# Kernel tuning notes

Measured on AMD Instinct MI355X. Metric: run time of the kernel, lower is better.

Reference implementation:

```python
import jax, jax.numpy as jnp
import numpy as np

B, S, HID = 2, 2048, 2048
H, KVH, D = 32, 4, 128
EPS = 1e-6
ROPE_THETA = 1e6
INIT = 0.02


def setup_inputs() -> dict:
    key = jax.random.key(0)
    ks = jax.random.split(key, 6)
    hidden_states = jax.random.normal(ks[0], (B, S, HID), jnp.float32)
    q_w = jax.random.normal(ks[1], (HID, H * D), jnp.float32) * INIT
    k_w = jax.random.normal(ks[2], (HID, KVH * D), jnp.float32) * INIT
    v_w = jax.random.normal(ks[3], (HID, KVH * D), jnp.float32) * INIT
    o_w = jax.random.normal(ks[4], (H * D, HID), jnp.float32) * INIT
    q_norm_w = jnp.ones((D,), jnp.float32)
    k_norm_w = jnp.ones((D,), jnp.float32)
    # rotary embeddings, computed once per position (B, S, D)
    pos = jnp.arange(S, dtype=jnp.float32)
    inv_freq = 1.0 / (ROPE_THETA ** (jnp.arange(0, D, 2, dtype=jnp.float32) / D))
    freqs = pos[:, None] * inv_freq[None, :]          # (S, D/2)
    emb = jnp.concatenate([freqs, freqs], axis=-1)    # (S, D)
    cos = jnp.broadcast_to(jnp.cos(emb)[None], (B, S, D))
    sin = jnp.broadcast_to(jnp.sin(emb)[None], (B, S, D))
    # causal mask (is_causal=True, sliding_window=None)
    attn_mask = jnp.tril(jnp.ones((S, S), bool))[None, None]  # (1,1,S,S)
    return {"hidden_states": hidden_states, "cos": cos, "sin": sin,
            "q_w": q_w, "k_w": k_w, "v_w": v_w, "o_w": o_w,
            "q_norm_w": q_norm_w, "k_norm_w": k_norm_w, "attn_mask": attn_mask}


def _rms_norm(x, w):
    xf = x.astype(jnp.float32)
    var = jnp.mean(jax.lax.square(xf), axis=-1, keepdims=True)
    return (w * (xf * jax.lax.rsqrt(var + EPS))).astype(x.dtype)


def _rotate_half(x):
    x1, x2 = jnp.split(x, 2, axis=-1)
    return jnp.concatenate([-x2, x1], axis=-1)


def _apply_rope(q, k, cos, sin):
    # q: (B,H,S,D), k: (B,KVH,S,D); cos/sin: (B,S,D) -> (B,1,S,D)
    cos = cos[:, None]
    sin = sin[:, None]
    q = q * cos + _rotate_half(q) * sin
    k = k * cos + _rotate_half(k) * sin
    return q, k


def reference(hidden_states, cos, sin, q_w, k_w, v_w, o_w, q_norm_w, k_norm_w, attn_mask):
    b, s, _ = hidden_states.shape
    scaling = D ** (-0.5)
    # projections + per-head QK RMSNorm
    q = _rms_norm((hidden_states @ q_w).reshape(b, s, H, D), q_norm_w)
    k = _rms_norm((hidden_states @ k_w).reshape(b, s, KVH, D), k_norm_w)
    v = (hidden_states @ v_w).reshape(b, s, KVH, D)
    q = jnp.transpose(q, (0, 2, 1, 3))   # (b,H,s,D)
    k = jnp.transpose(k, (0, 2, 1, 3))   # (b,KVH,s,D)
    v = jnp.transpose(v, (0, 2, 1, 3))
    q, k = _apply_rope(q, k, cos, sin)
    # GQA: repeat KV heads across groups
    groups = H // KVH
    k = jnp.repeat(k, groups, axis=1)    # (b,H,s,D)
    v = jnp.repeat(v, groups, axis=1)
    # eager softmax attention (fp32 softmax)
    scores = jnp.einsum('bhqd,bhkd->bhqk', q, k).astype(jnp.float32) * scaling
    scores = jnp.where(attn_mask, scores, jnp.float32(-1e30))
    probs = jax.nn.softmax(scores, axis=-1).astype(q.dtype)
    attn = jnp.einsum('bhqk,bhkd->bhqd', probs, v)
    attn = jnp.transpose(attn, (0, 2, 1, 3)).reshape(b, s, H * D)
    return attn @ o_w
```

## Files before the change

### kernel.cpp

```cpp
#include <hip/hip_runtime.h>
#include <hip/hip_bf16.h>

typedef unsigned short u16;
typedef __attribute__((ext_vector_type(4))) float f32x4;
typedef __attribute__((ext_vector_type(16))) float f32x16;
typedef __attribute__((ext_vector_type(8))) short bf16x8;
typedef __attribute__((ext_vector_type(4))) unsigned u32x4;

#define B_ 2
#define S_ 2048
#define HID_ 2048
#define H_ 32
#define KVH_ 4
#define D_ 128
#define M_ 4096
#define NQ_ 4096
#define NKV_ 512

typedef const __attribute__((address_space(1))) void gconst_void;
typedef __attribute__((address_space(3))) void lds_void;

static __device__ __forceinline__ void gload_lds16(const void* g, void* l) {
  __builtin_amdgcn_global_load_lds((gconst_void*)g, (lds_void*)l, 16, 0, 0);
}

static __device__ __forceinline__ u16 f2b(float f) {
  union { float f; unsigned i; } x; x.f = f;
  return (u16)((x.i + 0x7fffu + ((x.i >> 16) & 1u)) >> 16);
}
static __device__ __forceinline__ float b2f(u16 u) {
  union { unsigned i; float f; } x; x.i = ((unsigned)u) << 16;
  return x.f;
}

__global__ void k_cvt(const float* __restrict__ in, u16* __restrict__ out, int n4) {
  int i = blockIdx.x * blockDim.x + threadIdx.x;
  int stride = gridDim.x * blockDim.x;
  for (; i < n4; i += stride) {
    float4 v = reinterpret_cast<const float4*>(in)[i];
    ushort4 o;
    o.x = f2b(v.x); o.y = f2b(v.y); o.z = f2b(v.z); o.w = f2b(v.w);
    reinterpret_cast<ushort4*>(out)[i] = o;
  }
}

__global__ __launch_bounds__(256) void k_transpose(const float* __restrict__ W,
                                                   u16* __restrict__ Wt, int K, int N) {
  __shared__ u16 t[64][72];
  int n0 = blockIdx.x * 64, k0 = blockIdx.y * 64;
  int tid = threadIdx.x;
  int r = tid >> 4;
  int c4 = (tid & 15) * 4;
#pragma unroll
  for (int i = 0; i < 4; i++) {
    int k = r + i * 16;
    float4 v = *reinterpret_cast<const float4*>(W + (size_t)(k0 + k) * N + n0 + c4);
    t[k][c4 + 0] = f2b(v.x); t[k][c4 + 1] = f2b(v.y);
    t[k][c4 + 2] = f2b(v.z); t[k][c4 + 3] = f2b(v.w);
  }
  __syncthreads();
#pragma unroll
  for (int i = 0; i < 4; i++) {
    int n = r + i * 16;
    ushort4 o;
    o.x = t[c4 + 0][n]; o.y = t[c4 + 1][n]; o.z = t[c4 + 2][n]; o.w = t[c4 + 3][n];
    *reinterpret_cast<ushort4*>(Wt + (size_t)(n0 + n) * K + k0 + c4) = o;
  }
}

__device__ __forceinline__ void gemm_core(const u16* __restrict__ A, const u16* __restrict__ Bt,
                                          int K, int m0, int n0,
                                          u16* As, u16* Bs, f32x4 (&acc)[4][4]) {
  const int tid = threadIdx.x;
  const int lane = tid & 63;
  const int wid = tid >> 6;
  const int wr = wid >> 1, wc = wid & 1;
  const int lrow = lane & 15;
  const int hi = lane >> 4;
  const f32x4 zz = {0.f, 0.f, 0.f, 0.f};
#pragma unroll
  for (int i = 0; i < 4; i++)
#pragma unroll
    for (int j = 0; j < 4; j++) acc[i][j] = zz;

  const int srow = tid >> 3;
  const int sc16 = tid & 7;
  const int nk = K >> 6;
  int cur = 0;

#pragma unroll
  for (int rep = 0; rep < 4; rep++) {
    int row = rep * 32 + srow;
    int gcol = ((sc16 ^ (row & 7)) << 3);
    gload_lds16(A + (size_t)(m0 + row) * K + gcol, As + row * 64 + sc16 * 8);
    gload_lds16(Bt + (size_t)(n0 + row) * K + gcol, Bs + row * 64 + sc16 * 8);
  }
  __syncthreads();

  for (int t = 0; t < nk; t++) {
    if (t + 1 < nk) {
      int nxt = cur ^ 1;
      int kb = (t + 1) << 6;
#pragma unroll
      for (int rep = 0; rep < 4; rep++) {
        int row = rep * 32 + srow;
        int gcol = kb + ((sc16 ^ (row & 7)) << 3);
        gload_lds16(A + (size_t)(m0 + row) * K + gcol, As + nxt * 8192 + row * 64 + sc16 * 8);
        gload_lds16(Bt + (size_t)(n0 + row) * K + gcol, Bs + nxt * 8192 + row * 64 + sc16 * 8);
      }
    }
    const u16* Ac = As + cur * 8192;
    const u16* Bc = Bs + cur * 8192;
#pragma unroll
    for (int kc = 0; kc < 2; kc++) {
      bf16x8 af[4], bfr[4];
#pragma unroll
      for (int i = 0; i < 4; i++) {
        int row = wr * 64 + i * 16 + lrow;
        af[i] = *reinterpret_cast<const bf16x8*>(Ac + row * 64 + ((((kc << 2) + hi) ^ (row & 7)) << 3));
      }
#pragma unroll
      for (int j = 0; j < 4; j++) {
        int row = wc * 64 + j * 16 + lrow;
        bfr[j] = *reinterpret_cast<const bf16x8*>(Bc + row * 64 + ((((kc << 2) + hi) ^ (row & 7)) << 3));
      }
#pragma unroll
      for (int i = 0; i < 4; i++)
#pragma unroll
        for (int j = 0; j < 4; j++)
          acc[i][j] = __builtin_amdgcn_mfma_f32_16x16x32_bf16(af[i], bfr[j], acc[i][j], 0, 0, 0);
    }
    __syncthreads();
    cur ^= 1;
  }
}

__global__ __launch_bounds__(256, 2) void k_gemm_qkv(const u16* __restrict__ hb,
    const u16* __restrict__ qwt, const u16* __restrict__ kwt, const u16* __restrict__ vwt,
    u16* __restrict__ qb, u16* __restrict__ kb, u16* __restrict__ vb) {
  __shared__ u16 As[2 * 128 * 64], Bs[2 * 128 * 64];
  int mt = blockIdx.x, nt = blockIdx.y;
  const u16* Bt;
  if (nt < 32)      Bt = qwt;
  else if (nt < 36) Bt = kwt;
  else              Bt = vwt;
  int head = (nt < 32) ? nt : ((nt < 36) ? nt - 32 : nt - 36);
  f32x4 acc[4][4];
  gemm_core(hb, Bt, HID_, mt * 128, head * 128, As, Bs, acc);
  const int lane = threadIdx.x & 63;
  const int wid = threadIdx.x >> 6;
  const int wr = wid >> 1, wc = wid & 1;
  const int lr4 = (lane >> 4) * 4, lc = lane & 15;
#pragma unroll
  for (int i = 0; i < 4; i++)
#pragma unroll
    for (int j = 0; j < 4; j++)
#pragma unroll
      for (int r = 0; r < 4; r++) {
        int m = mt * 128 + wr * 64 + i * 16 + lr4 + r;
        int d = wc * 64 + j * 16 + lc;
        int b = m >> 11, s = m & (S_ - 1);
        u16 val = f2b(acc[i][j][r]);
        if (nt < 32) {
          qb[(((size_t)b * H_ + head) * S_ + s) * D_ + d] = val;
        } else if (nt < 36) {
          kb[(((size_t)b * KVH_ + head) * S_ + s) * D_ + d] = val;
        } else {
          vb[(((size_t)b * KVH_ + head) * D_ + d) * S_ + s] = val;
        }
      }
}

__global__ __launch_bounds__(256, 2) void k_gemm_o(const u16* __restrict__ ab,
    const u16* __restrict__ owt, float* __restrict__ out) {
  __shared__ u16 As[2 * 128 * 64], Bs[2 * 128 * 64];
  int mt = blockIdx.x, nt = blockIdx.y;
  f32x4 acc[4][4];
  gemm_core(ab, owt, NQ_, mt * 128, nt * 128, As, Bs, acc);
  const int lane = threadIdx.x & 63;
  const int wid = threadIdx.x >> 6;
  const int wr = wid >> 1, wc = wid & 1;
  const int lr4 = (lane >> 4) * 4, lc = lane & 15;
#pragma unroll
  for (int i = 0; i < 4; i++)
#pragma unroll
    for (int j = 0; j < 4; j++)
#pragma unroll
      for (int r = 0; r < 4; r++) {
        int m = mt * 128 + wr * 64 + i * 16 + lr4 + r;
        int n = nt * 128 + wc * 64 + j * 16 + lc;
        out[(size_t)m * HID_ + n] = acc[i][j][r];
      }
}

__global__ __launch_bounds__(256) void k_norm_rope(u16* __restrict__ qb, u16* __restrict__ kb,
    const float* __restrict__ cosp, const float* __restrict__ sinp,
    const float* __restrict__ qnw, const float* __restrict__ knw) {
  int row = blockIdx.x * 4 + (threadIdx.x >> 6);
  int lane = threadIdx.x & 63;
  const int QROWS = B_ * H_ * S_;
  u16* ptr; const float* nw; int b, s;
  if (row < QROWS) {
    ptr = qb + (size_t)row * D_; nw = qnw;
    s = row & (S_ - 1); b = row / (H_ * S_);
  } else {
    int r2 = row - QROWS;
    ptr = kb + (size_t)r2 * D_; nw = knw;
    s = r2 & (S_ - 1); b = r2 / (KVH_ * S_);
  }
  int d = lane * 2;
  float x0 = b2f(ptr[d]), x1 = b2f(ptr[d + 1]);
  float ss = x0 * x0 + x1 * x1;
#pragma unroll
  for (int m = 1; m < 64; m <<= 1) ss += __shfl_xor(ss, m);
  float inv = rsqrtf(ss * (1.0f / 128.0f) + 1e-6f);
  x0 = x0 * inv * nw[d]; x1 = x1 * inv * nw[d + 1];
  float p0 = __shfl_xor(x0, 32), p1 = __shfl_xor(x1, 32);
  float r0 = (lane < 32) ? -p0 : p0;
  float r1 = (lane < 32) ? -p1 : p1;
  const float* cp = cosp + ((size_t)b * S_ + s) * D_;
  const float* sp = sinp + ((size_t)b * S_ + s) * D_;
  ptr[d]     = f2b(x0 * cp[d]     + r0 * sp[d]);
  ptr[d + 1] = f2b(x1 * cp[d + 1] + r1 * sp[d + 1]);
}

__global__ __launch_bounds__(512, 2) void k_attn(const u16* __restrict__ q,
    const u16* __restrict__ k, const u16* __restrict__ vt, u16* __restrict__ out) {
  __shared__ u16 Kb[2 * 64 * 128];
  __shared__ u16 Vb[2 * 128 * 64];
  const int bh = blockIdx.y;
  const int b = bh >> 5, h = bh & 31;
  const int kvh = h >> 3;
  const int tid = threadIdx.x, lane = tid & 63, w = tid >> 6;
  const int lq = lane & 31, hi = lane >> 5;
  const u16* qp  = q  + ((size_t)(b * H_ + h) * S_) * D_;
  const u16* kp  = k  + ((size_t)(b * KVH_ + kvh) * S_) * D_;
  const u16* vtp = vt + ((size_t)(b * KVH_ + kvh) * D_) * S_;

  const int rowKa = tid >> 4;
  const int colK  = ((tid & 15) ^ (rowKa & 15)) << 3;
  const int rowVa = tid >> 3;
  const int colV  = ((tid & 7) ^ (rowVa & 7)) << 3;

  const float KSC = 0.08838834764831845f * 1.44269504088896340f;
  const f32x16 z16 = {0.f};

  int cur = 0;
  for (int half = 0; half < 2; half++) {
    const int qt = half ? (7 - (int)blockIdx.x) : (int)blockIdx.x;
    const int q0 = qt * 256;
    const int last = 4 * qt + 3;
    const int qg = q0 + 32 * w + lq;

    {
      u16* kd = Kb + cur * 8192 + tid * 8;
      u16* vd = Vb + cur * 8192 + tid * 8;
      gload_lds16(kp + (size_t)rowKa * D_ + colK, kd);
      gload_lds16(kp + (size_t)(rowKa + 32) * D_ + colK, kd + 4096);
      gload_lds16(vtp + (size_t)rowVa * S_ + colV, vd);
      gload_lds16(vtp + (size_t)(rowVa + 64) * S_ + colV, vd + 4096);
    }

    bf16x8 qf[8];
#pragma unroll
    for (int ds = 0; ds < 8; ds++)
      qf[ds] = *reinterpret_cast<const bf16x8*>(qp + (size_t)qg * D_ + ds * 16 + hi * 8);

    f32x16 oacc[4];
#pragma unroll
    for (int dt = 0; dt < 4; dt++) oacc[dt] = z16;
    float mrun = -1e30f, lrun = 0.f;

    __syncthreads();

    for (int nt = 0; nt <= last; nt++) {
      const int n0 = nt * 64;
      if (nt < last) {
        const int n1 = n0 + 64;
        u16* kd = Kb + (cur ^ 1) * 8192 + tid * 8;
        u16* vd = Vb + (cur ^ 1) * 8192 + tid * 8;
        gload_lds16(kp + (size_t)(n1 + rowKa) * D_ + colK, kd);
        gload_lds16(kp + (size_t)(n1 + rowKa + 32) * D_ + colK, kd + 4096);
        gload_lds16(vtp + (size_t)rowVa * S_ + n1 + colV, vd);
        gload_lds16(vtp + (size_t)(rowVa + 64) * S_ + n1 + colV, vd + 4096);
      }
      const u16* Kc = Kb + cur * 8192;
      const u16* Vc = Vb + cur * 8192;

      const bool skip = (n0 > q0 + 32 * w + 31);
      if (!skip) {
        const bool needmask = (n0 + 63 > q0 + 32 * w);

        f32x16 sacc[2];
        sacc[0] = z16; sacc[1] = z16;
#pragma unroll
        for (int ds = 0; ds < 8; ds++) {
          const int sl = (((ds << 1) + hi) ^ (lq & 15)) << 3;
          bf16x8 ka0 = *reinterpret_cast<const bf16x8*>(Kc + lq * 128 + sl);
          bf16x8 ka1 = *reinterpret_cast<const bf16x8*>(Kc + (lq + 32) * 128 + sl);
          __builtin_amdgcn_s_setprio(1);
          sacc[0] = __builtin_amdgcn_mfma_f32_32x32x16_bf16(ka0, qf[ds], sacc[0], 0, 0, 0);
          sacc[1] = __builtin_amdgcn_mfma_f32_32x32x16_bf16(ka1, qf[ds], sacc[1], 0, 0, 0);
          __builtin_amdgcn_s_setprio(0);
        }

        float tm = -1e30f;
#pragma unroll
        for (int t = 0; t < 2; t++)
#pragma unroll
          for (int r = 0; r < 16; r++) {
            float s2 = sacc[t][r] * KSC;
            if (needmask) {
              int kvg = n0 + 32 * t + (r & 3) + 8 * (r >> 2) + 4 * hi;
              if (kvg > qg) s2 = -1e30f;
            }
            sacc[t][r] = s2;
            tm = fmaxf(tm, s2);
          }
        tm = fmaxf(tm, __shfl_xor(tm, 32));
        if (__any(tm > mrun + 8.f)) {
          float mn = fmaxf(mrun, tm);
          float al = exp2f(mrun - mn);
          mrun = mn;
          lrun *= al;
#pragma unroll
          for (int r = 0; r < 16; r++) {
            float ar = __shfl(al, (r & 3) + 8 * (r >> 2) + 4 * hi);
#pragma unroll
            for (int dt = 0; dt < 4; dt++) oacc[dt][r] *= ar;
          }
        }
        float rs = 0.f;
#pragma unroll
        for (int t = 0; t < 2; t++)
#pragma unroll
          for (int r = 0; r < 16; r++) {
            float pv = exp2f(sacc[t][r] - mrun);
            sacc[t][r] = pv;
            rs += pv;
          }
        rs += __shfl_xor(rs, 32);
        lrun += rs;

        u32x4 pa[4];
#pragma unroll
        for (int t = 0; t < 2; t++)
#pragma unroll
          for (int ksl = 0; ksl < 2; ksl++) {
            unsigned wa, wb, wc2, wd;
            asm("v_cvt_pk_bf16_f32 %0, %1, %2" : "=v"(wa)
                : "v"(sacc[t][8 * ksl + 0]), "v"(sacc[t][8 * ksl + 1]));
            asm("v_cvt_pk_bf16_f32 %0, %1, %2" : "=v"(wb)
                : "v"(sacc[t][8 * ksl + 2]), "v"(sacc[t][8 * ksl + 3]));
            asm("v_cvt_pk_bf16_f32 %0, %1, %2" : "=v"(wc2)
                : "v"(sacc[t][8 * ksl + 4]), "v"(sacc[t][8 * ksl + 5]));
            asm("v_cvt_pk_bf16_f32 %0, %1, %2" : "=v"(wd)
                : "v"(sacc[t][8 * ksl + 6]), "v"(sacc[t][8 * ksl + 7]));
            asm("v_permlane32_swap_b32 %0, %1" : "+v"(wa), "+v"(wc2));
            asm("v_permlane32_swap_b32 %0, %1" : "+v"(wb), "+v"(wd));
            u32x4 t4 = {wa, wb, wc2, wd};
            pa[t * 2 + ksl] = t4;
          }

#pragma unroll
        for (int ks = 0; ks < 4; ks++) {
          bf16x8 paf = __builtin_bit_cast(bf16x8, pa[ks]);
          bf16x8 bv[4];
#pragma unroll
          for (int dt = 0; dt < 4; dt++) {
            int rowv = dt * 32 + lq;
            bv[dt] = *reinterpret_cast<const bf16x8*>(
                Vc + rowv * 64 + ((((ks << 1) + hi) ^ (rowv & 7)) << 3));
          }
          __builtin_amdgcn_s_setprio(1);
#pragma unroll
          for (int dt = 0; dt < 4; dt++)
            oacc[dt] = __builtin_amdgcn_mfma_f32_32x32x16_bf16(paf, bv[dt], oacc[dt], 0, 0, 0);
          __builtin_amdgcn_s_setprio(0);
        }
      }
      __syncthreads();
      cur ^= 1;
    }

    float linv = 1.0f / lrun;
#pragma unroll
    for (int r = 0; r < 16; r++) {
      const int idx_r = (r & 3) + 8 * (r >> 2) + 4 * hi;
      float lr = __shfl(linv, idx_r);
      size_t base = ((size_t)b * S_ + (q0 + 32 * w + idx_r)) * NQ_ + h * D_ + lq;
#pragma unroll
      for (int dt = 0; dt < 4; dt++)
        out[base + dt * 32] = f2b(oacc[dt][r] * lr);
    }
  }
}

extern "C" void kernel_launch(void* const* d_in, const int* in_sizes, int n_in,
                              void* d_out, int out_size, void* d_ws, size_t ws_size,
                              hipStream_t stream) {
  const float* hidden = (const float*)d_in[0];
  const float* cosp   = (const float*)d_in[1];
  const float* sinp   = (const float*)d_in[2];
  const float* q_w    = (const float*)d_in[3];
  const float* k_w    = (const float*)d_in[4];
  const float* v_w    = (const float*)d_in[5];
  const float* o_w    = (const float*)d_in[6];
  const float* qnw    = (const float*)d_in[7];
  const float* knw    = (const float*)d_in[8];

  char* p = (char*)d_ws;
  u16* hb  = (u16*)p; p += (size_t)M_ * HID_ * 2;
  u16* qwt = (u16*)p; p += (size_t)NQ_ * HID_ * 2;
  u16* kwt = (u16*)p; p += (size_t)NKV_ * HID_ * 2;
  u16* vwt = (u16*)p; p += (size_t)NKV_ * HID_ * 2;
  u16* owt = (u16*)p; p += (size_t)HID_ * NQ_ * 2;
  u16* qb  = (u16*)p; p += (size_t)B_ * H_ * S_ * D_ * 2;
  u16* kb  = (u16*)p; p += (size_t)B_ * KVH_ * S_ * D_ * 2;
  u16* vb  = (u16*)p; p += (size_t)B_ * KVH_ * S_ * D_ * 2;
  u16* ab  = (u16*)p; p += (size_t)M_ * NQ_ * 2;

  k_cvt<<<2048, 256, 0, stream>>>(hidden, hb, M_ * HID_ / 4);
  k_transpose<<<dim3(NQ_ / 64, HID_ / 64), 256, 0, stream>>>(q_w, qwt, HID_, NQ_);
  k_transpose<<<dim3(NKV_ / 64, HID_ / 64), 256, 0, stream>>>(k_w, kwt, HID_, NKV_);
  k_transpose<<<dim3(NKV_ / 64, HID_ / 64), 256, 0, stream>>>(v_w, vwt, HID_, NKV_);
  k_transpose<<<dim3(HID_ / 64, NQ_ / 64), 256, 0, stream>>>(o_w, owt, NQ_, HID_);
  k_gemm_qkv<<<dim3(M_ / 128, 40), 256, 0, stream>>>(hb, qwt, kwt, vwt, qb, kb, vb);
  k_norm_rope<<<(B_ * H_ * S_ + B_ * KVH_ * S_) / 4, 256, 0, stream>>>(qb, kb, cosp, sinp, qnw, knw);
  k_attn<<<dim3(4, B_ * H_), 512, 0, stream>>>(qb, kb, vb, ab);
  k_gemm_o<<<dim3(M_ / 128, HID_ / 128), 256, 0, stream>>>(ab, owt, (float*)d_out);
}
```

Baseline: 371.8 us.

## Add 256x256 8-wave Q-projection GEMM and XCD-aware block remapping

Moves the Q projection out of the combined QKV GEMM into a dedicated kernel. It uses 256x256 tiles, 512 threads, quadrant-wise LDS double buffering with explicit waitcnt and barriers, and MFMA priority boosting, so each loaded tile is reused across more output. K/V projection stays in its own smaller kernel. The QKV, attention and output-projection grids become 1D with a swizzle that maps consecutive blocks onto the same XCD, aiming to improve L2 locality. The cost is more kernel launches, higher register and LDS pressure in the new GEMM, and delicate hand-tuned vmcnt synchronization.

```diff
diff --git a/kernel.cpp b/kernel.cpp
--- a/kernel.cpp
+++ b/kernel.cpp
@@ -23,6 +23,9 @@
 static __device__ __forceinline__ void gload_lds16(const void* g, void* l) {
   __builtin_amdgcn_global_load_lds((gconst_void*)g, (lds_void*)l, 16, 0, 0);
 }
+
+#define WAITV(N) asm volatile("s_waitcnt vmcnt(" #N ")" ::: "memory")
+#define WAITL0() asm volatile("s_waitcnt lgkmcnt(0)" ::: "memory")
 
 static __device__ __forceinline__ u16 f2b(float f) {
   union { float f; unsigned i; } x; x.f = f;
@@ -135,16 +138,145 @@
   }
 }
 
-__global__ __launch_bounds__(256, 2) void k_gemm_qkv(const u16* __restrict__ hb,
-    const u16* __restrict__ qwt, const u16* __restrict__ kwt, const u16* __restrict__ vwt,
-    u16* __restrict__ qb, u16* __restrict__ kb, u16* __restrict__ vb) {
+__global__ __launch_bounds__(512, 2) void k_gemm_q8(const u16* __restrict__ A,
+    const u16* __restrict__ Bt, u16* __restrict__ qb) {
+  __shared__ u16 Ash[2][2][128 * 64];
+  __shared__ u16 Bsh[2][2][128 * 64];
+  const int bid = blockIdx.x;
+  const int wg = (bid & 7) * 32 + (bid >> 3);
+  const int mt = wg & 15, nt = wg >> 4;
+  const int m0 = mt * 256, n0 = nt * 256;
+  const int K = HID_, nk = K >> 6;
+  const int tid = threadIdx.x, lane = tid & 63;
+  const int wv = tid >> 6, wr = wv >> 2, wc = wv & 3;
+  const int lrow = lane & 15, hi4 = lane >> 4;
+
+  const int s0r = tid >> 3, sc = tid & 7;
+  const int s1r = (tid + 512) >> 3;
+
+  auto stgA = [&](int h, int t, int d) {
+    gload_lds16(A + (size_t)(m0 + h * 128 + s0r) * K + t * 64 + ((sc ^ (s0r & 7)) << 3),
+                &Ash[d][h][s0r * 64 + sc * 8]);
+    gload_lds16(A + (size_t)(m0 + h * 128 + s1r) * K + t * 64 + ((sc ^ (s1r & 7)) << 3),
+                &Ash[d][h][s1r * 64 + sc * 8]);
+  };
+  auto stgB = [&](int h, int t, int d) {
+    gload_lds16(Bt + (size_t)(n0 + h * 128 + s0r) * K + t * 64 + ((sc ^ (s0r & 7)) << 3),
+                &Bsh[d][h][s0r * 64 + sc * 8]);
+    gload_lds16(Bt + (size_t)(n0 + h * 128 + s1r) * K + t * 64 + ((sc ^ (s1r & 7)) << 3),
+                &Bsh[d][h][s1r * 64 + sc * 8]);
+  };
+
+  f32x4 acc[8][4];
+  const f32x4 zz = {0.f, 0.f, 0.f, 0.f};
+#pragma unroll
+  for (int f = 0; f < 8; f++)
+#pragma unroll
+    for (int j = 0; j < 4; j++) acc[f][j] = zz;
+
+  bf16x8 af[4][2], bfr[2][2];
+
+  auto lda = [&](int mh, int d) {
+#pragma unroll
+    for (int fi = 0; fi < 4; fi++) {
+      int row = fi * 32 + wr * 16 + lrow;
+#pragma unroll
+      for (int kk = 0; kk < 2; kk++)
+        af[fi][kk] = *reinterpret_cast<const bf16x8*>(
+            &Ash[d][mh][row * 64 + ((((kk << 2) + hi4) ^ (row & 7)) << 3)]);
+    }
+  };
+  auto ldb = [&](int nh, int d) {
+#pragma unroll
+    for (int ji = 0; ji < 2; ji++) {
+      int row = ji * 64 + wc * 16 + lrow;
+#pragma unroll
+      for (int kk = 0; kk < 2; kk++)
+        bfr[ji][kk] = *reinterpret_cast<const bf16x8*>(
+            &Bsh[d][nh][row * 64 + ((((kk << 2) + hi4) ^ (row & 7)) << 3)]);
+    }
+  };
+  auto mq = [&](int mh, int nh) {
+    __builtin_amdgcn_s_setprio(1);
+#pragma unroll
+    for (int kk = 0; kk < 2; kk++)
+#pragma unroll
+      for (int fi = 0; fi < 4; fi++)
+#pragma unroll
+        for (int ji = 0; ji < 2; ji++)
+          acc[mh * 4 + fi][nh * 2 + ji] = __builtin_amdgcn_mfma_f32_16x16x32_bf16(
+              af[fi][kk], bfr[ji][kk], acc[mh * 4 + fi][nh * 2 + ji], 0, 0, 0);
+    __builtin_amdgcn_s_setprio(0);
+  };
+
+  stgA(0, 0, 0); stgB(0, 0, 0); stgA(1, 0, 0); stgB(1, 0, 0);
+  WAITV(0);
+  __builtin_amdgcn_s_barrier();
+
+  for (int t = 0; t < nk; t++) {
+    const int d = t & 1, nd = d ^ 1;
+    const bool pre = (t + 1 < nk);
+    if (pre) { stgA(0, t + 1, nd); stgB(0, t + 1, nd); }
+    lda(0, d); ldb(0, d);
+    WAITV(6);
+    __builtin_amdgcn_sched_barrier(0);
+    __builtin_amdgcn_s_barrier();
+    WAITL0();
+    __builtin_amdgcn_sched_barrier(0);
+    mq(0, 0);
+    __builtin_amdgcn_s_barrier();
+    if (pre) stgA(1, t + 1, nd);
+    lda(1, d);
+    WAITV(6);
+    __builtin_amdgcn_sched_barrier(0);
+    __builtin_amdgcn_s_barrier();
+    WAITL0();
+    __builtin_amdgcn_sched_barrier(0);
+    mq(1, 0);
+    __builtin_amdgcn_s_barrier();
+    if (pre) stgB(1, t + 1, nd);
+    ldb(1, d);
+    __builtin_amdgcn_sched_barrier(0);
+    __builtin_amdgcn_s_barrier();
+    WAITL0();
+    __builtin_amdgcn_sched_barrier(0);
+    mq(1, 1);
+    __builtin_amdgcn_s_barrier();
+    lda(0, d);
+    WAITV(4);
+    __builtin_amdgcn_sched_barrier(0);
+    __builtin_amdgcn_s_barrier();
+    WAITL0();
+    __builtin_amdgcn_sched_barrier(0);
+    mq(0, 1);
+    __builtin_amdgcn_s_barrier();
+  }
+
+  const int lr4 = hi4 * 4, lc = lane & 15;
+#pragma unroll
+  for (int f = 0; f < 8; f++)
+#pragma unroll
+    for (int j = 0; j < 4; j++)
+#pragma unroll
+      for (int rr = 0; rr < 4; rr++) {
+        int m = m0 + f * 32 + wr * 16 + lr4 + rr;
+        int ncol = n0 + j * 64 + wc * 16 + lc;
+        int b = m >> 11, s = m & (S_ - 1);
+        int head = ncol >> 7, dd = ncol & 127;
+        qb[(((size_t)b * H_ + head) * S_ + s) * D_ + dd] = f2b(acc[f][j][rr]);
+      }
+}
+
+__global__ __launch_bounds__(256, 2) void k_gemm_kv(const u16* __restrict__ hb,
+    const u16* __restrict__ kwt, const u16* __restrict__ vwt,
+    u16* __restrict__ kb, u16* __restrict__ vb) {
   __shared__ u16 As[2 * 128 * 64], Bs[2 * 128 * 64];
-  int mt = blockIdx.x, nt = blockIdx.y;
-  const u16* Bt;
-  if (nt < 32)      Bt = qwt;
-  else if (nt < 36) Bt = kwt;
-  else              Bt = vwt;
-  int head = (nt < 32) ? nt : ((nt < 36) ? nt - 32 : nt - 36);
+  const int bid = blockIdx.x;
+  const int wg = (bid & 7) * 32 + (bid >> 3);
+  const int mt = wg & 31, nt = wg >> 5;
+  const bool isv = nt >= 4;
+  const int head = isv ? nt - 4 : nt;
+  const u16* Bt = isv ? vwt : kwt;
   f32x4 acc[4][4];
   gemm_core(hb, Bt, HID_, mt * 128, head * 128, As, Bs, acc);
   const int lane = threadIdx.x & 63;
@@ -161,20 +293,17 @@
         int d = wc * 64 + j * 16 + lc;
         int b = m >> 11, s = m & (S_ - 1);
         u16 val = f2b(acc[i][j][r]);
-        if (nt < 32) {
-          qb[(((size_t)b * H_ + head) * S_ + s) * D_ + d] = val;
-        } else if (nt < 36) {
-          kb[(((size_t)b * KVH_ + head) * S_ + s) * D_ + d] = val;
-        } else {
-          vb[(((size_t)b * KVH_ + head) * D_ + d) * S_ + s] = val;
-        }
+        if (isv) vb[(((size_t)b * KVH_ + head) * D_ + d) * S_ + s] = val;
+        else     kb[(((size_t)b * KVH_ + head) * S_ + s) * D_ + d] = val;
       }
 }
 
 __global__ __launch_bounds__(256, 2) void k_gemm_o(const u16* __restrict__ ab,
     const u16* __restrict__ owt, float* __restrict__ out) {
   __shared__ u16 As[2 * 128 * 64], Bs[2 * 128 * 64];
-  int mt = blockIdx.x, nt = blockIdx.y;
+  const int bid = blockIdx.x;
+  const int wg = (bid & 7) * 64 + (bid >> 3);
+  const int mt = wg & 31, nt = wg >> 5;
   f32x4 acc[4][4];
   gemm_core(ab, owt, NQ_, mt * 128, nt * 128, As, Bs, acc);
   const int lane = threadIdx.x & 63;
@@ -228,7 +357,9 @@
     const u16* __restrict__ k, const u16* __restrict__ vt, u16* __restrict__ out) {
   __shared__ u16 Kb[2 * 64 * 128];
   __shared__ u16 Vb[2 * 128 * 64];
-  const int bh = blockIdx.y;
+  const int bid = blockIdx.x;
+  const int wg = (bid & 7) * 32 + (bid >> 3);
+  const int qx = wg & 3, bh = wg >> 2;
   const int b = bh >> 5, h = bh & 31;
   const int kvh = h >> 3;
   const int tid = threadIdx.x, lane = tid & 63, w = tid >> 6;
@@ -247,7 +378,7 @@
 
   int cur = 0;
   for (int half = 0; half < 2; half++) {
-    const int qt = half ? (7 - (int)blockIdx.x) : (int)blockIdx.x;
+    const int qt = half ? (7 - qx) : qx;
     const int q0 = qt * 256;
     const int last = 4 * qt + 3;
     const int qg = q0 + 32 * w + lq;
@@ -425,8 +556,9 @@
   k_transpose<<<dim3(NKV_ / 64, HID_ / 64), 256, 0, stream>>>(k_w, kwt, HID_, NKV_);
   k_transpose<<<dim3(NKV_ / 64, HID_ / 64), 256, 0, stream>>>(v_w, vwt, HID_, NKV_);
   k_transpose<<<dim3(HID_ / 64, NQ_ / 64), 256, 0, stream>>>(o_w, owt, NQ_, HID_);
-  k_gemm_qkv<<<dim3(M_ / 128, 40), 256, 0, stream>>>(hb, qwt, kwt, vwt, qb, kb, vb);
+  k_gemm_q8<<<256, 512, 0, stream>>>(hb, qwt, qb);
+  k_gemm_kv<<<256, 256, 0, stream>>>(hb, kwt, vwt, kb, vb);
   k_norm_rope<<<(B_ * H_ * S_ + B_ * KVH_ * S_) / 4, 256, 0, stream>>>(qb, kb, cosp, sinp, qnw, knw);
-  k_attn<<<dim3(4, B_ * H_), 512, 0, stream>>>(qb, kb, vb, ab);
-  k_gemm_o<<<dim3(M_ / 128, HID_ / 128), 256, 0, stream>>>(ab, owt, (float*)d_out);
-}
+  k_attn<<<256, 512, 0, stream>>>(qb, kb, vb, ab);
+  k_gemm_o<<<512, 256, 0, stream>>>(ab, owt, (float*)d_out);
+}
```

Measured after the change: 361.2 us. 1.03x faster.
